# Kernel optimization log

Measured on AMD Instinct MI355X. Metric: run time of the kernel, lower is better.

## Reference

```python
import jax, jax.numpy as jnp
import numpy as np

EMBED_DIM = 1024
EXPAND_RATIO = 128  # head_dim; n_heads = EMBED_DIM // EXPAND_RATIO = 8
B, N = 4, 2048


def setup_inputs() -> dict:
    key = jax.random.key(0)
    ks = jax.random.split(key, 6)
    std = 0.02
    d = EMBED_DIM
    return {
        "x": jax.random.normal(ks[0], (B, N, d), dtype=jnp.float32),
        "Wq": jax.random.normal(ks[1], (d, d), dtype=jnp.float32) * std,
        "Wk": jax.random.normal(ks[2], (d, d), dtype=jnp.float32) * std,
        "Wv": jax.random.normal(ks[3], (d, d), dtype=jnp.float32) * std,
        "Wo": jax.random.normal(ks[4], (d, d), dtype=jnp.float32) * std,
        "norm_w": jnp.ones((d,), dtype=jnp.float32),
    }


def _rmsnorm(x, w, eps=1e-6):
    return x * jax.lax.rsqrt(jnp.mean(x * x, axis=-1, keepdims=True) + eps) * w


def _gla_scan(q, k, v, g):
    # q,k,v,g: [b, n, h, d]; state S: [b, h, d_k, d_v]
    b, n, h, d = q.shape
    qs, ks_, vs, gs = (jnp.moveaxis(t, 1, 0) for t in (q, k, v, g))  # [n,b,h,d]
    S0 = jnp.zeros((b, h, d, d), dtype=q.dtype)

    def step(S, inp):
        q_t, k_t, v_t, g_t = inp
        # S_t = diag(exp(g_t)) S_{t-1} + k_t^T v_t (gate on key dim)
        S = jnp.exp(g_t)[..., :, None] * S + k_t[..., :, None] * v_t[..., None, :]
        o_t = jnp.einsum('bhk,bhkv->bhv', q_t, S)
        return S, o_t

    _, outs = jax.lax.scan(step, S0, (qs, ks_, vs, gs))
    return jnp.moveaxis(outs, 0, 1)  # [b, n, h, d]


def reference(x, Wq, Wk, Wv, Wo, norm_w):
    b, n, D = x.shape
    hd = EXPAND_RATIO
    h = D // hd

    q = jax.nn.silu(x @ Wq.T)          # q_activation = silu
    f = jax.nn.sigmoid(x @ Wk.T)       # f = sigmoid(k_proj(x))
    log_f = jax.nn.log_sigmoid(f)      # faithful: logsigmoid applied to f (lower_bound=None path)
    k = 1.0 - f
    v = x @ Wv.T

    def split_heads(t):
        return t.reshape(b, n, h, hd)

    out = _gla_scan(split_heads(q), split_heads(k), split_heads(v), split_heads(log_f))
    out = out.reshape(b, n, D)
    out = _rmsnorm(out, norm_w)        # norm_pos='ogate', no output gate
    return out @ Wo.T
```

## Files before the change

kernel.cpp:

```cpp
#include <hip/hip_runtime.h>
#include <cstdint>
#include <cstddef>


typedef unsigned short u16;
using f32x4  = __attribute__((ext_vector_type(4))) float;
using bf16x8 = __attribute__((ext_vector_type(8))) short;

__device__ __forceinline__ float bf2f(u16 u) {
  union { unsigned int i; float f; } v; v.i = ((unsigned int)u) << 16; return v.f;
}
__device__ __forceinline__ u16 f2bf(float f) {
  union { float f; unsigned int i; } v; v.f = f;
  unsigned int r = v.i + 0x7fffu + ((v.i >> 16) & 1u);
  return (u16)(r >> 16);
}
__device__ __forceinline__ void async_load16(const void* g, void* l) {
  __builtin_amdgcn_global_load_lds(
      (const __attribute__((address_space(1))) unsigned int*)(uintptr_t)g,
      (__attribute__((address_space(3))) unsigned int*)(uintptr_t)l, 16, 0, 0);
}
__device__ __forceinline__ float logsig01(float f) {
  float u = f * f;
  return -0.69314718f + 0.5f * f + u * (-0.125f + u * (0.0052083335f - u * 3.472222e-4f));
}

__device__ __forceinline__ void gemm128_core(const u16* __restrict__ Ag, const u16* __restrict__ Bg,
                                             u16* smem, f32x4 (&acc)[4][4]) {
  const int tid = threadIdx.x;
  const int lane = tid & 63, wave = tid >> 6;
  const int wm = (wave & 1) * 64, wn = (wave >> 1) * 64;
  const int r = lane & 15, quad = lane >> 4;
  const int xk = r & 3;
  const u16* baseA = smem + (wm + r) * 32 + ((quad ^ xk) & 3) * 8;
  const u16* baseB = smem + 4096 + (wn + r) * 32 + ((quad ^ xk) & 3) * 8;
  const int soff = (tid >> 2) * 1024 + (((tid & 3) ^ ((tid >> 2) & 3)) * 8);
  u16* dA = smem + wave * 512;
  u16* dB = smem + 4096 + wave * 512;
#pragma unroll
  for (int it = 0; it < 2; ++it) {
    async_load16(Ag + it * 65536 + soff, dA + it * 2048);
    async_load16(Bg + it * 65536 + soff, dB + it * 2048);
  }
#pragma unroll 2
  for (int kt = 0; kt < 32; ++kt) {
    const int cb = (kt & 1) * 8192;
    __syncthreads();
    if (kt < 31) {
      const int nb = ((kt + 1) & 1) * 8192;
      const u16* As = Ag + (kt + 1) * 32 + soff;
      const u16* Bs = Bg + (kt + 1) * 32 + soff;
#pragma unroll
      for (int it = 0; it < 2; ++it) {
        async_load16(As + it * 65536, dA + nb + it * 2048);
        async_load16(Bs + it * 65536, dB + nb + it * 2048);
      }
    }
    bf16x8 af[4], bv[4];
#pragma unroll
    for (int i = 0; i < 4; ++i) af[i] = *(const bf16x8*)(baseA + cb + i * 512);
#pragma unroll
    for (int j = 0; j < 4; ++j) bv[j] = *(const bf16x8*)(baseB + cb + j * 512);
#pragma unroll
    for (int i = 0; i < 4; ++i)
#pragma unroll
      for (int j = 0; j < 4; ++j)
        acc[i][j] = __builtin_amdgcn_mfma_f32_16x16x32_bf16(af[i], bv[j], acc[i][j], 0, 0, 0);
  }
}

__global__ __launch_bounds__(256) void cast_all(
    const float* __restrict__ x, const float* __restrict__ w0, const float* __restrict__ w1,
    const float* __restrict__ w2, const float* __restrict__ w3, const float* __restrict__ nw,
    u16* __restrict__ xd, u16* __restrict__ d0, u16* __restrict__ d1,
    u16* __restrict__ d2, u16* __restrict__ d3, float* __restrict__ Sv) {
  const int blk = blockIdx.x;
  if (blk >= 12288) {
    Sv[(blk - 12288) * 256 + threadIdx.x] = 0.f;
    return;
  }
  const float* src;
  u16* dst;
  int i;
  bool fold = false;
  if (blk < 8192) {
    src = x; dst = xd; i = blk * 256 + threadIdx.x;
  } else {
    int wb = blk - 8192, which = wb >> 10;
    i = (wb & 1023) * 256 + threadIdx.x;
    src = which == 0 ? w0 : (which == 1 ? w1 : (which == 2 ? w2 : w3));
    dst = which == 0 ? d0 : (which == 1 ? d1 : (which == 2 ? d2 : d3));
    fold = (which == 3);
  }
  float4 v = ((const float4*)src)[i];
  if (fold) {
    float4 wv = ((const float4*)nw)[i & 255];
    v.x *= wv.x; v.y *= wv.y; v.z *= wv.z; v.w *= wv.w;
  }
  unsigned int lo = (unsigned)f2bf(v.x) | ((unsigned)f2bf(v.y) << 16);
  unsigned int hi = (unsigned)f2bf(v.z) | ((unsigned)f2bf(v.w) << 16);
  ((uint2*)dst)[i] = make_uint2(lo, hi);
}

__global__ __launch_bounds__(256) void hgru_gemm_qkv(
    const u16* __restrict__ Xb, const u16* __restrict__ Wqb, const u16* __restrict__ Wkb,
    const u16* __restrict__ Wvb, u16* __restrict__ Qb, u16* __restrict__ Kb,
    u16* __restrict__ Vb) {
  __shared__ alignas(16) u16 smem[16384];
  const int which = blockIdx.y >> 3, bn = blockIdx.y & 7;
  const u16* W = which == 0 ? Wqb : (which == 1 ? Wkb : Wvb);
  const u16* Ag = Xb + (size_t)blockIdx.x * 128 * 1024;
  const u16* Bg = W + (size_t)bn * 128 * 1024;
  f32x4 acc[4][4] = {};
  gemm128_core(Ag, Bg, smem, acc);
  const int tid = threadIdx.x, lane = tid & 63, wave = tid >> 6;
  const int wm = (wave & 1) * 64, wn = (wave >> 1) * 64;
  const int r = lane & 15, quad = lane >> 4;
#pragma unroll
  for (int i = 0; i < 4; ++i)
#pragma unroll
    for (int j = 0; j < 4; ++j)
#pragma unroll
      for (int reg = 0; reg < 4; ++reg) {
        int m = blockIdx.x * 128 + wm + i * 16 + quad * 4 + reg;
        int n = bn * 128 + wn + j * 16 + r;
        size_t off = (size_t)m * 1024 + n;
        float z = acc[i][j][reg];
        if (which == 0) {
          Qb[off] = f2bf(z / (1.f + __expf(-z)));
        } else if (which == 1) {
          float ek = __expf(-z);
          Kb[off] = f2bf(ek / (1.f + ek));
        } else {
          Vb[off] = f2bf(z);
        }
      }
}

__global__ __launch_bounds__(256, 4) void hgru_scan(
    const u16* __restrict__ Qg, const u16* __restrict__ Kg, const u16* __restrict__ Vg,
    u16* __restrict__ O, float* __restrict__ Ssum) {
  __shared__ alignas(16) char smem[40448];
  u16* sKt  = (u16*)(smem);
  u16* sVt1 = (u16*)(smem + 10240);
  u16* sK   = (u16*)(smem + 15360);
  u16* sQ   = (u16*)(smem + 24064);
  u16* sVt2 = (u16*)(smem + 32768);
  u16* sAm  = (u16*)(smem + 37888);
  u16* sU   = (u16*)(smem);
  u16* sO   = (u16*)(smem + 17408);

  const int tid = threadIdx.x, blk = blockIdx.x;
  const int vh = blk & 1, c = (blk >> 1) & 63, bh = blk >> 7, h = bh & 7, bb_ = bh >> 3;
  const size_t rb = (size_t)(bb_ * 2048 + c * 32) * 1024 + h * 128;
  const bool haveP = (c > 0);
  const size_t rb1 = haveP ? rb - 32 * 1024 : rb;

  const int lane = tid & 63, wave = tid >> 6;
  const int r = lane & 15, quad = lane >> 4;
  const int ts = tid & 31, g8 = tid >> 5;

  uint4 V2 = *(const uint4*)(Vg + rb  + (size_t)ts * 1024 + vh * 64 + g8 * 8);
  uint4 V1 = *(const uint4*)(Vg + rb1 + (size_t)ts * 1024 + vh * 64 + g8 * 8);
  { const u16* vp = (const u16*)&V2;
#pragma unroll
    for (int e = 0; e < 8; ++e) sVt2[(g8 * 8 + e) * 40 + ts] = vp[e]; }
  if (haveP) {
    const u16* vp = (const u16*)&V1;
#pragma unroll
    for (int e = 0; e < 8; ++e) sVt1[(g8 * 8 + e) * 40 + ts] = vp[e];
  }

  const int col = tid & 127;
  if (tid < 128) {
    if (haveP) {
      const u16* kc = Kg + rb1 + col;
      unsigned int kraw[16];
      float bC = 0.f;
#pragma unroll
      for (int t = 0; t < 16; ++t) {
        unsigned int a = kc[(size_t)(2 * t) * 1024];
        unsigned int b = kc[(size_t)(2 * t + 1) * 1024];
        kraw[t] = a | (b << 16);
        bC += logsig01(1.f - bf2f((u16)a)) + logsig01(1.f - bf2f((u16)b));
      }
      float run = 0.f;
#pragma unroll
      for (int t = 0; t < 16; ++t) {
        float ka = bf2f((u16)(kraw[t] & 0xffff));
        float kb = bf2f((u16)(kraw[t] >> 16));
        run += logsig01(1.f - ka);
        sKt[col * 40 + 2 * t]     = f2bf(ka * __expf(bC - run));
        run += logsig01(1.f - kb);
        sKt[col * 40 + 2 * t + 1] = f2bf(kb * __expf(bC - run));
      }
    }
  } else {
    const u16* kc = Kg + rb + col;
    const u16* qc = Qg + rb + col;
    float run = 0.f;
#pragma unroll
    for (int t = 0; t < 32; ++t) {
      u16 ku = kc[(size_t)t * 1024];
      u16 qu = qc[(size_t)t * 1024];
      float kv = bf2f(ku);
      run += logsig01(1.f - kv);
      sQ[t * 136 + col] = f2bf(bf2f(qu) * __expf(run));
      sK[t * 136 + col] = f2bf(kv * __expf(-run));
    }
  }
  __syncthreads();

  f32x4 accU[2][4] = {};
  const int vm = (wave & 1) * 32, in = (wave >> 1) * 64;
  if (haveP) {
#pragma unroll
    for (int mi = 0; mi < 2; ++mi) {
      bf16x8 af = *(const bf16x8*)(sVt1 + (vm + mi * 16 + r) * 40 + quad * 8);
#pragma unroll
      for (int nj = 0; nj < 4; ++nj) {
        bf16x8 bv = *(const bf16x8*)(sKt + (in + nj * 16 + r) * 40 + quad * 8);
        accU[mi][nj] = __builtin_amdgcn_mfma_f32_16x16x32_bf16(af, bv, accU[mi][nj], 0, 0, 0);
      }
    }
  }
  { const int mi = wave & 1, nj = wave >> 1;
    f32x4 a1 = {0.f, 0.f, 0.f, 0.f};
#pragma unroll
    for (int ks = 0; ks < 4; ++ks) {
      bf16x8 af = *(const bf16x8*)(sQ + (mi * 16 + r) * 136 + ks * 32 + quad * 8);
      bf16x8 bk = *(const bf16x8*)(sK + (nj * 16 + r) * 136 + ks * 32 + quad * 8);
      a1 = __builtin_amdgcn_mfma_f32_16x16x32_bf16(af, bk, a1, 0, 0, 0);
    }
#pragma unroll
    for (int reg = 0; reg < 4; ++reg) {
      int t = mi * 16 + quad * 4 + reg, s = nj * 16 + r;
      sAm[t * 40 + s] = (s <= t) ? f2bf(a1[reg]) : (u16)0;
    } }
  __syncthreads();

  if (haveP) {
#pragma unroll
    for (int mi = 0; mi < 2; ++mi)
#pragma unroll
      for (int nj = 0; nj < 4; ++nj)
#pragma unroll
        for (int reg = 0; reg < 4; ++reg) {
          int vl = vm + mi * 16 + quad * 4 + reg;
          int i  = in + nj * 16 + r;
          sU[vl * 136 + i] = f2bf(accU[mi][nj][reg]);
        }
  }
  __syncthreads();

  { const int mi = wave & 1, no = (wave >> 1) * 32;
    bf16x8 af0 = *(const bf16x8*)(sAm + (mi * 16 + r) * 40 + quad * 8);
    bf16x8 afq[4];
    if (haveP) {
#pragma unroll
      for (int ks = 0; ks < 4; ++ks)
        afq[ks] = *(const bf16x8*)(sQ + (mi * 16 + r) * 136 + ks * 32 + quad * 8);
    }
    f32x4 ssq = {0.f, 0.f, 0.f, 0.f};
#pragma unroll
    for (int j = 0; j < 2; ++j) {
      f32x4 acc2 = {0.f, 0.f, 0.f, 0.f};
      bf16x8 bv0 = *(const bf16x8*)(sVt2 + (no + j * 16 + r) * 40 + quad * 8);
      acc2 = __builtin_amdgcn_mfma_f32_16x16x32_bf16(af0, bv0, acc2, 0, 0, 0);
      if (haveP) {
#pragma unroll
        for (int ks = 0; ks < 4; ++ks) {
          bf16x8 bs = *(const bf16x8*)(sU + (no + j * 16 + r) * 136 + ks * 32 + quad * 8);
          acc2 = __builtin_amdgcn_mfma_f32_16x16x32_bf16(afq[ks], bs, acc2, 0, 0, 0);
        }
      }
      ssq += acc2 * acc2;
#pragma unroll
      for (int reg = 0; reg < 4; ++reg) {
        int t = mi * 16 + quad * 4 + reg;
        sO[t * 72 + no + j * 16 + r] = f2bf(acc2[reg]);
      }
    }
    const int rowg = bb_ * 2048 + c * 32 + mi * 16 + quad * 4;
#pragma unroll
    for (int reg = 0; reg < 4; ++reg) {
      float v = ssq[reg];
      v += __shfl_xor(v, 1); v += __shfl_xor(v, 2);
      v += __shfl_xor(v, 4); v += __shfl_xor(v, 8);
      if (r == 0) atomicAdd(&Ssum[rowg + reg], v);
    } }
  __syncthreads();

  { const int row = tid >> 3, seg = tid & 7;
    *(uint4*)(O + rb + (size_t)row * 1024 + vh * 64 + seg * 8) =
        *(const uint4*)(sO + row * 72 + seg * 8); }
}

__global__ __launch_bounds__(256) void hgru_gemm_out(const u16* __restrict__ Ab,
                                                     const u16* __restrict__ Wob,
                                                     const float* __restrict__ Ssum,
                                                     float* __restrict__ out) {
  __shared__ alignas(16) u16 smem[16384];
  const u16* Ag = Ab + (size_t)blockIdx.x * 128 * 1024;
  const u16* Bg = Wob + (size_t)blockIdx.y * 128 * 1024;
  f32x4 acc[4][4] = {};
  gemm128_core(Ag, Bg, smem, acc);
  const int tid = threadIdx.x, lane = tid & 63, wave = tid >> 6;
  const int wm = (wave & 1) * 64, wn = (wave >> 1) * 64;
  const int r = lane & 15, quad = lane >> 4;
#pragma unroll
  for (int i = 0; i < 4; ++i)
#pragma unroll
    for (int reg = 0; reg < 4; ++reg) {
      int m = blockIdx.x * 128 + wm + i * 16 + quad * 4 + reg;
      float sm = rsqrtf(Ssum[m] * (1.f / 1024.f) + 1e-6f);
#pragma unroll
      for (int j = 0; j < 4; ++j) {
        int n = blockIdx.y * 128 + wn + j * 16 + r;
        out[(size_t)m * 1024 + n] = acc[i][j][reg] * sm;
      }
    }
}

extern "C" void kernel_launch(void* const* d_in, const int* in_sizes, int n_in,
                              void* d_out, int out_size, void* d_ws, size_t ws_size,
                              hipStream_t stream) {
  const float* x  = (const float*)d_in[0];
  const float* Wq = (const float*)d_in[1];
  const float* Wk = (const float*)d_in[2];
  const float* Wv = (const float*)d_in[3];
  const float* Wo = (const float*)d_in[4];
  const float* nw = (const float*)d_in[5];
  float* out = (float*)d_out;
  char* ws = (char*)d_ws;

  u16* Xb   = (u16*)(ws + 0);
  u16* Wqb  = (u16*)(ws + 16777216);
  u16* Wkb  = (u16*)(ws + 18874368);
  u16* Wvb  = (u16*)(ws + 20971520);
  u16* Wob  = (u16*)(ws + 23068672);
  u16* Qb   = (u16*)(ws + 25165824);
  u16* Kb   = (u16*)(ws + 41943040);
  u16* Vb   = (u16*)(ws + 58720256);
  u16* Obf  = (u16*)(ws + 75497472);
  float* Sv = (float*)(ws + 92274688);

  cast_all<<<12320, 256, 0, stream>>>(x, Wq, Wk, Wv, Wo, nw, Xb, Wqb, Wkb, Wvb, Wob, Sv);

  dim3 gq(64, 24);
  hgru_gemm_qkv<<<gq, 256, 0, stream>>>(Xb, Wqb, Wkb, Wvb, Qb, Kb, Vb);
  hgru_scan<<<4096, 256, 0, stream>>>(Qb, Kb, Vb, Obf, Sv);
  dim3 go(64, 8);
  hgru_gemm_out<<<go, 256, 0, stream>>>(Obf, Wob, Sv, out);
}
```

Measured before the change: 221.9 us.

## Rewrite QKV GEMM with 256x256 tiles, 8 waves, and ping-pong async LDS pipeline

Replaces the 128x128, 4-wave QKV projection GEMM with a 256x256-tile, 512-thread kernel that double-buffers A and B in 128 KB of LDS using async global-to-LDS loads interleaved with MFMA phases. It uses s_setprio and barriers to stagger compute and loads, and remaps block IDs for better L2 locality. The goal is higher operand reuse and better overlap of memory with MFMA. The cost is much larger LDS use, only 384 blocks, and tight waitcnt bookkeeping that could stall or race.

```diff
diff --git a/kernel.cpp b/kernel.cpp
--- a/kernel.cpp
+++ b/kernel.cpp
@@ -102,38 +102,149 @@
   ((uint2*)dst)[i] = make_uint2(lo, hi);
 }
 
-__global__ __launch_bounds__(256) void hgru_gemm_qkv(
+__global__ __launch_bounds__(512, 2) void hgru_gemm_qkv8(
     const u16* __restrict__ Xb, const u16* __restrict__ Wqb, const u16* __restrict__ Wkb,
     const u16* __restrict__ Wvb, u16* __restrict__ Qb, u16* __restrict__ Kb,
     u16* __restrict__ Vb) {
-  __shared__ alignas(16) u16 smem[16384];
-  const int which = blockIdx.y >> 3, bn = blockIdx.y & 7;
-  const u16* W = which == 0 ? Wqb : (which == 1 ? Wkb : Wvb);
-  const u16* Ag = Xb + (size_t)blockIdx.x * 128 * 1024;
-  const u16* Bg = W + (size_t)bn * 128 * 1024;
-  f32x4 acc[4][4] = {};
-  gemm128_core(Ag, Bg, smem, acc);
-  const int tid = threadIdx.x, lane = tid & 63, wave = tid >> 6;
-  const int wm = (wave & 1) * 64, wn = (wave >> 1) * 64;
+  __shared__ alignas(16) u16 smem[65536];
+  const int tid = threadIdx.x;
+  const int bid = blockIdx.x;
+  const int wg = (bid & 7) * 48 + (bid >> 3);
+  const int bm = wg / 12, bn = wg % 12;
+  const int which = bn >> 2;
+  const u16* __restrict__ Ag = Xb + (size_t)bm * 256 * 1024;
+  const u16* __restrict__ Wm = which == 0 ? Wqb : (which == 1 ? Wkb : Wvb);
+  const u16* __restrict__ Bg = Wm + (size_t)(bn & 3) * 256 * 1024;
+
+  const int lane = tid & 63, wave = tid >> 6;
+  const int wr = wave >> 2, wc = wave & 3;
   const int r = lane & 15, quad = lane >> 4;
-#pragma unroll
-  for (int i = 0; i < 4; ++i)
-#pragma unroll
-    for (int j = 0; j < 4; ++j)
+
+  const int srow = tid >> 3;
+  const int scol = ((tid & 7) ^ (srow & 7)) * 8;
+  const u16* aS = Ag + (size_t)srow * 1024 + scol;
+  const u16* bS = Bg + (size_t)srow * 1024 + scol;
+  u16* aD = smem + wave * 512;
+  u16* bD = smem + 32768 + wave * 512;
+
+  auto stageA = [&](int c, int kt, int h) {
+    async_load16(aS + (h * 128) * 1024 + kt * 64,      aD + c * 16384 + h * 8192);
+    async_load16(aS + (h * 128 + 64) * 1024 + kt * 64, aD + c * 16384 + h * 8192 + 4096);
+  };
+  auto stageB = [&](int c, int kt, int h) {
+    async_load16(bS + (h * 128) * 1024 + kt * 64,      bD + c * 16384 + h * 8192);
+    async_load16(bS + (h * 128 + 64) * 1024 + kt * 64, bD + c * 16384 + h * 8192 + 4096);
+  };
+
+  const int ch0 = (quad ^ (r & 7)) * 8;
+  const int ch1 = ((4 | quad) ^ (r & 7)) * 8;
+  const u16* aR = smem + (wr * 128 + r) * 64;
+  const u16* bR = smem + 32768 + (wc * 64 + r) * 64;
+
+  f32x4 acc[8][4] = {};
+  bf16x8 a[4][2], b[4][2];
+
+  stageB(0, 0, 0); stageB(0, 0, 1);
+  stageA(0, 0, 0); stageA(0, 0, 1);
+  stageB(1, 1, 0); stageB(1, 1, 1);
+  asm volatile("s_waitcnt vmcnt(4)" ::: "memory");
+  __builtin_amdgcn_s_barrier();
+
+  for (int kt = 0; kt < 16; ++kt) {
+    const int c = kt & 1, co = c * 16384;
+
+#pragma unroll
+    for (int mi = 0; mi < 4; ++mi) {
+      a[mi][0] = *(const bf16x8*)(aR + co + mi * 1024 + ch0);
+      a[mi][1] = *(const bf16x8*)(aR + co + mi * 1024 + ch1);
+    }
+#pragma unroll
+    for (int nj = 0; nj < 2; ++nj) {
+      b[nj][0] = *(const bf16x8*)(bR + co + nj * 1024 + ch0);
+      b[nj][1] = *(const bf16x8*)(bR + co + nj * 1024 + ch1);
+    }
+    if (kt + 1 < 16) stageA(c ^ 1, kt + 1, 0);
+    __builtin_amdgcn_s_barrier();
+    __builtin_amdgcn_s_setprio(1);
+#pragma unroll
+    for (int mi = 0; mi < 4; ++mi)
+#pragma unroll
+      for (int nj = 0; nj < 2; ++nj) {
+        acc[mi][nj] = __builtin_amdgcn_mfma_f32_16x16x32_bf16(a[mi][0], b[nj][0], acc[mi][nj], 0, 0, 0);
+        acc[mi][nj] = __builtin_amdgcn_mfma_f32_16x16x32_bf16(a[mi][1], b[nj][1], acc[mi][nj], 0, 0, 0);
+      }
+    __builtin_amdgcn_s_setprio(0);
+    __builtin_amdgcn_s_barrier();
+
+#pragma unroll
+    for (int nj = 2; nj < 4; ++nj) {
+      b[nj][0] = *(const bf16x8*)(bR + co + nj * 1024 + ch0);
+      b[nj][1] = *(const bf16x8*)(bR + co + nj * 1024 + ch1);
+    }
+    if (kt + 1 < 16) stageA(c ^ 1, kt + 1, 1);
+    __builtin_amdgcn_s_barrier();
+    __builtin_amdgcn_s_setprio(1);
+#pragma unroll
+    for (int mi = 0; mi < 4; ++mi)
+#pragma unroll
+      for (int nj = 2; nj < 4; ++nj) {
+        acc[mi][nj] = __builtin_amdgcn_mfma_f32_16x16x32_bf16(a[mi][0], b[nj][0], acc[mi][nj], 0, 0, 0);
+        acc[mi][nj] = __builtin_amdgcn_mfma_f32_16x16x32_bf16(a[mi][1], b[nj][1], acc[mi][nj], 0, 0, 0);
+      }
+    __builtin_amdgcn_s_setprio(0);
+    __builtin_amdgcn_s_barrier();
+
+#pragma unroll
+    for (int mi = 0; mi < 4; ++mi) {
+      a[mi][0] = *(const bf16x8*)(aR + co + (mi + 4) * 1024 + ch0);
+      a[mi][1] = *(const bf16x8*)(aR + co + (mi + 4) * 1024 + ch1);
+    }
+    if (kt + 2 < 16) stageB(c, kt + 2, 0);
+    __builtin_amdgcn_s_barrier();
+    __builtin_amdgcn_s_setprio(1);
+#pragma unroll
+    for (int mi = 0; mi < 4; ++mi)
+#pragma unroll
+      for (int nj = 0; nj < 2; ++nj) {
+        acc[mi + 4][nj] = __builtin_amdgcn_mfma_f32_16x16x32_bf16(a[mi][0], b[nj][0], acc[mi + 4][nj], 0, 0, 0);
+        acc[mi + 4][nj] = __builtin_amdgcn_mfma_f32_16x16x32_bf16(a[mi][1], b[nj][1], acc[mi + 4][nj], 0, 0, 0);
+      }
+    __builtin_amdgcn_s_setprio(0);
+    __builtin_amdgcn_s_barrier();
+
+    if (kt + 2 < 16) stageB(c, kt + 2, 1);
+    __builtin_amdgcn_s_barrier();
+    __builtin_amdgcn_s_setprio(1);
+#pragma unroll
+    for (int mi = 0; mi < 4; ++mi)
+#pragma unroll
+      for (int nj = 2; nj < 4; ++nj) {
+        acc[mi + 4][nj] = __builtin_amdgcn_mfma_f32_16x16x32_bf16(a[mi][0], b[nj][0], acc[mi + 4][nj], 0, 0, 0);
+        acc[mi + 4][nj] = __builtin_amdgcn_mfma_f32_16x16x32_bf16(a[mi][1], b[nj][1], acc[mi + 4][nj], 0, 0, 0);
+      }
+    __builtin_amdgcn_s_setprio(0);
+    if (kt < 14)       asm volatile("s_waitcnt vmcnt(4)" ::: "memory");
+    else if (kt == 14) asm volatile("s_waitcnt vmcnt(0)" ::: "memory");
+    __builtin_amdgcn_s_barrier();
+  }
+
+  u16* __restrict__ dst = which == 0 ? Qb : (which == 1 ? Kb : Vb);
+  const int nbase = (bn & 3) * 256 + wc * 64;
+  const int mbase = bm * 256 + wr * 128 + quad * 4;
+#pragma unroll
+  for (int mi = 0; mi < 8; ++mi)
+#pragma unroll
+    for (int nj = 0; nj < 4; ++nj)
 #pragma unroll
       for (int reg = 0; reg < 4; ++reg) {
-        int m = blockIdx.x * 128 + wm + i * 16 + quad * 4 + reg;
-        int n = bn * 128 + wn + j * 16 + r;
-        size_t off = (size_t)m * 1024 + n;
-        float z = acc[i][j][reg];
-        if (which == 0) {
-          Qb[off] = f2bf(z / (1.f + __expf(-z)));
-        } else if (which == 1) {
-          float ek = __expf(-z);
-          Kb[off] = f2bf(ek / (1.f + ek));
-        } else {
-          Vb[off] = f2bf(z);
-        }
+        int m = mbase + mi * 16 + reg;
+        int n = nbase + nj * 16 + r;
+        float z = acc[mi][nj][reg];
+        float v;
+        if (which == 0)      v = z / (1.f + __expf(-z));
+        else if (which == 1) { float ek = __expf(-z); v = ek / (1.f + ek); }
+        else                 v = z;
+        dst[(size_t)m * 1024 + n] = f2bf(v);
       }
 }
 
@@ -347,8 +458,7 @@
 
   cast_all<<<12320, 256, 0, stream>>>(x, Wq, Wk, Wv, Wo, nw, Xb, Wqb, Wkb, Wvb, Wob, Sv);
 
-  dim3 gq(64, 24);
-  hgru_gemm_qkv<<<gq, 256, 0, stream>>>(Xb, Wqb, Wkb, Wvb, Qb, Kb, Vb);
+  hgru_gemm_qkv8<<<384, 512, 0, stream>>>(Xb, Wqb, Wkb, Wvb, Qb, Kb, Vb);
   hgru_scan<<<4096, 256, 0, stream>>>(Qb, Kb, Vb, Obf, Sv);
   dim3 go(64, 8);
   hgru_gemm_out<<<go, 256, 0, stream>>>(Obf, Wob, Sv, out);
```

Measured after the change: 227.2 us. +2.4%, slower.
